# Kernel tuning notes

Measured on AMD Instinct MI355X. Metric: run time of the kernel, lower is better.

Reference implementation:

```python
import jax, jax.numpy as jnp
import numpy as np

L, C = 256, 20
BATCH = 1024


def _pairwise_mask(L, C, mask_type='pairwise'):
    # mask[l1, c1, l2, c2] nonzero iff positions interact (l2 - l1 >= 1, or == 1 for neighbor)
    ls = jnp.arange(L)
    d = ls[None, :] - ls[:, None]  # [L, L] = l2 - l1
    m = (d >= 1) if mask_type == 'pairwise' else (d == 1)
    return jnp.broadcast_to(m[:, None, :, None], (L, C, L, C)).astype(jnp.float32)


def setup_inputs() -> dict:
    key = jax.random.key(0)
    k1, k2, k3 = jax.random.split(key, 3)
    x_lc = jax.random.uniform(k1, (BATCH, L * C), dtype=jnp.float32)
    theta_0 = jnp.zeros((1,), dtype=jnp.float32)
    theta_lc = jax.random.normal(k2, (L, C), dtype=jnp.float32) / np.sqrt(L)
    theta_lclc = jax.random.normal(k3, (L, C, L, C), dtype=jnp.float32) / np.sqrt(L * L)
    return {"x_lc": x_lc, "theta_0": theta_0, "theta_lc": theta_lc, "theta_lclc": theta_lclc}


def reference(x_lc, theta_0, theta_lc, theta_lclc):
    Ld, Cd = theta_lc.shape
    mask = _pairwise_mask(Ld, Cd, 'pairwise')
    # additive term: sum_lc theta_lc * x_lc  -> [B, 1]
    lin = x_lc @ theta_lc.reshape(Ld * Cd)  # [B]
    # pairwise term: x^T (theta * mask) x, expressed as a masked GEMM instead of a
    # broadcasted [B, L, C, L, C] product
    Theta = (theta_lclc * mask).reshape(Ld * Cd, Ld * Cd)  # [LC, LC]
    xm = x_lc @ Theta  # [B, LC]
    quad = jnp.sum(xm * x_lc, axis=1)  # [B]
    phi = theta_0 + (lin + quad)[:, None]  # [B, 1]
    return phi
```

## Files before the change

### kernel.cpp

```cpp
#include <hip/hip_runtime.h>
#include <hip/hip_bf16.h>
#include <cstdint>
#include <cstddef>

#define LCN 5120
#define BN  1024
#define CN  20
#define TP  65

typedef __attribute__((ext_vector_type(4))) float  floatx4;
typedef __attribute__((ext_vector_type(8))) short  shortx8;
typedef __attribute__((ext_vector_type(4))) unsigned short ushortx4;
typedef __attribute__((ext_vector_type(8))) unsigned short ushortx8;

static __device__ __forceinline__ unsigned short f2bf(float f) {
    __hip_bfloat16 h = __float2bfloat16(f);
    return *reinterpret_cast<unsigned short*>(&h);
}

static __device__ __forceinline__ void gload_lds16(const void* g, void* l) {
    __builtin_amdgcn_global_load_lds(
        (const __attribute__((address_space(1))) void*)g,
        (__attribute__((address_space(3))) void*)l,
        16, 0, 0);
}

__global__ __launch_bounds__(256) void k_theta(const float* __restrict__ th,
                                               unsigned short* __restrict__ Tt) {
    const int i0 = blockIdx.x * 64;
    const int j0 = blockIdx.y * 64;
    const int lmax = (128 * (i0 / 128) + 127) / CN;
    const int ch   = (CN * lmax + 511) / 512;
    if (j0 >= ch * 512) return;

    __shared__ unsigned short Ts[64 * TP];
    const int t = threadIdx.x;
    const int c = t & 15, r = t >> 4;
#pragma unroll
    for (int rr = 0; rr < 4; ++rr) {
        const int j  = j0 + rr * 16 + r;
        const int lj = j / CN;
        const floatx4 v = *reinterpret_cast<const floatx4*>(th + (size_t)j * LCN + i0 + c * 4);
#pragma unroll
        for (int e = 0; e < 4; ++e) {
            const int li = (i0 + c * 4 + e) / CN;
            Ts[(rr * 16 + r) * TP + c * 4 + e] = (li > lj) ? f2bf(v[e]) : (unsigned short)0;
        }
    }
    __syncthreads();
    const int c2 = t & 7, r2 = t >> 3;
#pragma unroll
    for (int ww = 0; ww < 2; ++ww) {
        const int il = ww * 32 + r2;
        ushortx8 o;
#pragma unroll
        for (int e = 0; e < 8; ++e) o[e] = Ts[(c2 * 8 + e) * TP + il];
        *reinterpret_cast<ushortx8*>(Tt + (size_t)(i0 + il) * LCN + j0 + c2 * 8) = o;
    }
}

__global__ __launch_bounds__(256) void k_init(const float* __restrict__ x,
                                              const float* __restrict__ th0,
                                              const float* __restrict__ thlc,
                                              float* __restrict__ out,
                                              unsigned short* __restrict__ Xb) {
    const int b = blockIdx.x;
    const int tid = threadIdx.x;
    const floatx4* xr = reinterpret_cast<const floatx4*>(x + (size_t)b * LCN);
    const floatx4* tr = reinterpret_cast<const floatx4*>(thlc);
    ushortx4* xw = reinterpret_cast<ushortx4*>(Xb + (size_t)b * LCN);
    float s = 0.0f;
    for (int k = tid; k < LCN / 4; k += 256) {
        const floatx4 a = xr[k], t2 = tr[k];
        s += a[0] * t2[0] + a[1] * t2[1] + a[2] * t2[2] + a[3] * t2[3];
        ushortx4 o;
#pragma unroll
        for (int e = 0; e < 4; ++e) o[e] = f2bf(a[e]);
        xw[k] = o;
    }
#pragma unroll
    for (int off = 32; off > 0; off >>= 1) s += __shfl_down(s, off, 64);
    __shared__ float ws4[4];
    if ((tid & 63) == 0) ws4[tid >> 6] = s;
    __syncthreads();
    if (tid == 0) out[b] = th0[0] + ws4[0] + ws4[1] + ws4[2] + ws4[3];
}

__global__ __launch_bounds__(256) void k_quad(
    const unsigned short* __restrict__ Xb,
    const unsigned short* __restrict__ Tt,
    float*                __restrict__ out,
    const int tot)
{
    const int bid  = blockIdx.x;
    const int xcd  = bid & 7;
    const int slot = bid >> 3;
    const int m    = slot & 7;
    const int g    = slot >> 3;
    int q = g * 8 + xcd;
    if (q >= tot) return;

    __shared__ unsigned short As[128 * 32];
    __shared__ unsigned short Bs[128 * 32];
    __shared__ float partial[128];

    const int tid  = threadIdx.x;
    const int lane = tid & 63;
    const int w    = tid >> 6;
    const int wm   = w & 1;
    const int wn   = w >> 1;
    const int lrow = lane & 15;
    const int kq   = lane >> 4;

    int n = 0, c = 0;
    for (int t = 0; t < 40; ++t) {
        const int lmax = (128 * t + 127) / CN;
        const int chn  = (CN * lmax + 511) / 512;
        if (q < chn) { n = t; c = q; break; }
        q -= chn;
    }
    const int b0 = m * 128;
    const int n0 = n * 128;
    const int k0 = c * 512;

    if (tid < 128) partial[tid] = 0.0f;

    floatx4 acc[4][4];
#pragma unroll
    for (int mt = 0; mt < 4; ++mt)
#pragma unroll
        for (int nt = 0; nt < 4; ++nt) acc[mt][nt] = (floatx4)0.0f;

    int aoff[4], boff[4];
#pragma unroll
    for (int mt = 0; mt < 4; ++mt) {
        const int row = wm * 64 + mt * 16 + lrow;
        aoff[mt] = row * 32 + (((kq + (row >> 1)) & 3) << 3);
    }
#pragma unroll
    for (int nt = 0; nt < 4; ++nt) {
        const int row = wn * 64 + nt * 16 + lrow;
        boff[nt] = row * 32 + (((kq + (row >> 1)) & 3) << 3);
    }

    for (int kk = 0; kk < 16; ++kk) {
        const int kc = k0 + kk * 32;
#pragma unroll
        for (int t = 0; t < 2; ++t) {
            const int s    = t * 256 + tid;
            const int row  = s >> 2;
            const int gseg = ((s & 3) - (row >> 1)) & 3;
            char* la = (char*)As + (size_t)(t * 256 + w * 64) * 16;
            char* lb = (char*)Bs + (size_t)(t * 256 + w * 64) * 16;
            gload_lds16(Xb + (size_t)(b0 + row) * LCN + kc + gseg * 8, la);
            gload_lds16(Tt + (size_t)(n0 + row) * LCN + kc + gseg * 8, lb);
        }
        __syncthreads();

        shortx8 af[4], bfr[4];
#pragma unroll
        for (int mt = 0; mt < 4; ++mt)
            af[mt] = *reinterpret_cast<const shortx8*>(As + aoff[mt]);
#pragma unroll
        for (int nt = 0; nt < 4; ++nt)
            bfr[nt] = *reinterpret_cast<const shortx8*>(Bs + boff[nt]);
#pragma unroll
        for (int mt = 0; mt < 4; ++mt)
#pragma unroll
            for (int nt = 0; nt < 4; ++nt)
                acc[mt][nt] = __builtin_amdgcn_mfma_f32_16x16x32_bf16(af[mt], bfr[nt], acc[mt][nt], 0, 0, 0);
        __syncthreads();
    }

#pragma unroll
    for (int mt = 0; mt < 4; ++mt) {
#pragma unroll
        for (int r = 0; r < 4; ++r) {
            const int b = b0 + wm * 64 + mt * 16 + kq * 4 + r;
            float s = 0.0f;
#pragma unroll
            for (int nt = 0; nt < 4; ++nt) {
                const int i = n0 + wn * 64 + nt * 16 + lrow;
                const __hip_bfloat16 hv = *reinterpret_cast<const __hip_bfloat16*>(&Xb[(size_t)b * LCN + i]);
                s += acc[mt][nt][r] * __bfloat162float(hv);
            }
            s += __shfl_xor(s, 1, 64);
            s += __shfl_xor(s, 2, 64);
            s += __shfl_xor(s, 4, 64);
            s += __shfl_xor(s, 8, 64);
            if (lrow == 0) atomicAdd(&partial[b - b0], s);
        }
    }
    __syncthreads();
    if (tid < 128) atomicAdd(&out[b0 + tid], partial[tid]);
}

extern "C" void kernel_launch(void* const* d_in, const int* in_sizes, int n_in,
                              void* d_out, int out_size, void* d_ws, size_t ws_size,
                              hipStream_t stream) {
    const float* x      = (const float*)d_in[0];
    const float* th0    = (const float*)d_in[1];
    const float* thlc   = (const float*)d_in[2];
    const float* thlclc = (const float*)d_in[3];
    float* out = (float*)d_out;

    unsigned short* Tt = (unsigned short*)d_ws;
    unsigned short* Xb = (unsigned short*)((char*)d_ws + (size_t)LCN * LCN * 2);

    k_theta<<<dim3(LCN / 64, LCN / 64), 256, 0, stream>>>(thlclc, Tt);
    k_init<<<dim3(BN), 256, 0, stream>>>(x, th0, thlc, out, Xb);

    int tot = 0;
    for (int t = 0; t < 40; ++t) {
        const int lmax = (128 * t + 127) / CN;
        tot += (CN * lmax + 511) / 512;
    }
    const int groups = (tot + 7) / 8;
    k_quad<<<dim3(groups * 64), 256, 0, stream>>>(Xb, Tt, out, tot);
}
```

Before: 232.0 us.

## Use the transposed quadratic form to drop the LDS transpose of theta

The quadratic form x^T Θ x equals x^T Θ^T x, so the theta matrix can be consumed in its natural row-major layout. The LDS-based transpose kernel is replaced by a simple coalesced elementwise fp32-to-bf16 conversion that applies the mask and skips chunks below the diagonal. The k_quad chunk enumeration is rewritten so each output row tile iterates over the K chunks above its diagonal rather than below it. This removes the strided shared-memory transpose from the preprocessing pass, while the amount of GEMM work stays roughly the same.

Measured after the change: 233.5 us. About the same (+0.6%).

```diff
diff --git a/kernel.cpp b/kernel.cpp
--- a/kernel.cpp
+++ b/kernel.cpp
@@ -6,12 +6,10 @@
 #define LCN 5120
 #define BN  1024
 #define CN  20
-#define TP  65
 
 typedef __attribute__((ext_vector_type(4))) float  floatx4;
 typedef __attribute__((ext_vector_type(8))) short  shortx8;
 typedef __attribute__((ext_vector_type(4))) unsigned short ushortx4;
-typedef __attribute__((ext_vector_type(8))) unsigned short ushortx8;
 
 static __device__ __forceinline__ unsigned short f2bf(float f) {
     __hip_bfloat16 h = __float2bfloat16(f);
@@ -25,38 +23,21 @@
         16, 0, 0);
 }
 
-__global__ __launch_bounds__(256) void k_theta(const float* __restrict__ th,
-                                               unsigned short* __restrict__ Tt) {
-    const int i0 = blockIdx.x * 64;
-    const int j0 = blockIdx.y * 64;
-    const int lmax = (128 * (i0 / 128) + 127) / CN;
-    const int ch   = (CN * lmax + 511) / 512;
-    if (j0 >= ch * 512) return;
-
-    __shared__ unsigned short Ts[64 * TP];
-    const int t = threadIdx.x;
-    const int c = t & 15, r = t >> 4;
-#pragma unroll
-    for (int rr = 0; rr < 4; ++rr) {
-        const int j  = j0 + rr * 16 + r;
-        const int lj = j / CN;
-        const floatx4 v = *reinterpret_cast<const floatx4*>(th + (size_t)j * LCN + i0 + c * 4);
-#pragma unroll
-        for (int e = 0; e < 4; ++e) {
-            const int li = (i0 + c * 4 + e) / CN;
-            Ts[(rr * 16 + r) * TP + c * 4 + e] = (li > lj) ? f2bf(v[e]) : (unsigned short)0;
-        }
-    }
-    __syncthreads();
-    const int c2 = t & 7, r2 = t >> 3;
-#pragma unroll
-    for (int ww = 0; ww < 2; ++ww) {
-        const int il = ww * 32 + r2;
-        ushortx8 o;
-#pragma unroll
-        for (int e = 0; e < 8; ++e) o[e] = Ts[(c2 * 8 + e) * TP + il];
-        *reinterpret_cast<ushortx8*>(Tt + (size_t)(i0 + il) * LCN + j0 + c2 * 8) = o;
-    }
+__global__ __launch_bounds__(256) void k_conv(const float* __restrict__ th,
+                                              unsigned short* __restrict__ Tn) {
+    const int a  = blockIdx.y;
+    const int t  = a >> 7;
+    const int c0 = (CN * ((128 * t) / CN + 1)) / 512;
+    const int bx = blockIdx.x;
+    if (2 * (bx + 1) <= c0) return;
+    const int kmin = CN * (a / CN + 1);
+    const int col  = bx * 1024 + threadIdx.x * 4;
+    const floatx4 v = *reinterpret_cast<const floatx4*>(th + (size_t)a * LCN + col);
+    ushortx4 o;
+#pragma unroll
+    for (int e = 0; e < 4; ++e)
+        o[e] = (col + e >= kmin) ? f2bf(v[e]) : (unsigned short)0;
+    *reinterpret_cast<ushortx4*>(Tn + (size_t)a * LCN + col) = o;
 }
 
 __global__ __launch_bounds__(256) void k_init(const float* __restrict__ x,
@@ -88,7 +69,7 @@
 
 __global__ __launch_bounds__(256) void k_quad(
     const unsigned short* __restrict__ Xb,
-    const unsigned short* __restrict__ Tt,
+    const unsigned short* __restrict__ Tn,
     float*                __restrict__ out,
     const int tot)
 {
@@ -114,9 +95,9 @@
 
     int n = 0, c = 0;
     for (int t = 0; t < 40; ++t) {
-        const int lmax = (128 * t + 127) / CN;
-        const int chn  = (CN * lmax + 511) / 512;
-        if (q < chn) { n = t; c = q; break; }
+        const int c0t = (CN * ((128 * t) / CN + 1)) / 512;
+        const int chn = 10 - c0t;
+        if (q < chn) { n = t; c = c0t + q; break; }
         q -= chn;
     }
     const int b0 = m * 128;
@@ -153,7 +134,7 @@
             char* la = (char*)As + (size_t)(t * 256 + w * 64) * 16;
             char* lb = (char*)Bs + (size_t)(t * 256 + w * 64) * 16;
             gload_lds16(Xb + (size_t)(b0 + row) * LCN + kc + gseg * 8, la);
-            gload_lds16(Tt + (size_t)(n0 + row) * LCN + kc + gseg * 8, lb);
+            gload_lds16(Tn + (size_t)(n0 + row) * LCN + kc + gseg * 8, lb);
         }
         __syncthreads();
 
@@ -180,8 +161,8 @@
             float s = 0.0f;
 #pragma unroll
             for (int nt = 0; nt < 4; ++nt) {
-                const int i = n0 + wn * 64 + nt * 16 + lrow;
-                const __hip_bfloat16 hv = *reinterpret_cast<const __hip_bfloat16*>(&Xb[(size_t)b * LCN + i]);
+                const int a = n0 + wn * 64 + nt * 16 + lrow;
+                const __hip_bfloat16 hv = *reinterpret_cast<const __hip_bfloat16*>(&Xb[(size_t)b * LCN + a]);
                 s += acc[mt][nt][r] * __bfloat162float(hv);
             }
             s += __shfl_xor(s, 1, 64);
@@ -204,17 +185,17 @@
     const float* thlclc = (const float*)d_in[3];
     float* out = (float*)d_out;
 
-    unsigned short* Tt = (unsigned short*)d_ws;
+    unsigned short* Tn = (unsigned short*)d_ws;
     unsigned short* Xb = (unsigned short*)((char*)d_ws + (size_t)LCN * LCN * 2);
 
-    k_theta<<<dim3(LCN / 64, LCN / 64), 256, 0, stream>>>(thlclc, Tt);
+    k_conv<<<dim3(LCN / 1024, LCN), 256, 0, stream>>>(thlclc, Tn);
     k_init<<<dim3(BN), 256, 0, stream>>>(x, th0, thlc, out, Xb);
 
     int tot = 0;
     for (int t = 0; t < 40; ++t) {
-        const int lmax = (128 * t + 127) / CN;
-        tot += (CN * lmax + 511) / 512;
+        const int c0t = (CN * ((128 * t) / CN + 1)) / 512;
+        tot += 10 - c0t;
     }
     const int groups = (tot + 7) / 8;
-    k_quad<<<dim3(groups * 64), 256, 0, stream>>>(Xb, Tt, out, tot);
-}
+    k_quad<<<dim3(groups * 64), 256, 0, stream>>>(Xb, Tn, out, tot);
+}
```
